# Optimization experiments

Hardware: AMD Instinct MI355X
Metric: run time of the kernel (lower is better)

## Reference

```python
import jax, jax.numpy as jnp
import numpy as np

EPS = 1e-07
B, C, K = 524288, 42, 8  # batch, n_channel, n_constituent
HID = [5, 4, 4]


def _make_net_params(key, n_in, lower=-1.0, upper=1.0):
    dims = [n_in] + HID + [3]
    params = []
    for i in range(4):
        key, kw, kb = jax.random.split(key, 3)
        W = jax.random.uniform(kw, (C, dims[i + 1], dims[i]), minval=lower, maxval=upper)
        if i < 3:  # hidden bias init 0.9..1.1
            b = jax.random.uniform(kb, (C, dims[i + 1]), minval=0.9, maxval=1.1)
        else:     # output bias init -0.1..0.1
            b = jax.random.uniform(kb, (C, dims[i + 1]), minval=-0.1, maxval=0.1)
        params.append(W)
        params.append(b)
    return params


def setup_inputs() -> dict:
    key = jax.random.key(0)
    k = jax.random.split(key, 6)
    inp = {
        'tau': jax.random.uniform(k[0], (B, C, K), dtype=jnp.float32),
        'mu_direct': jax.random.uniform(k[1], (B, 1), minval=0.01, maxval=1.0, dtype=jnp.float32),
        'mu_diffuse': jax.random.uniform(k[2], (B, 1), minval=0.01, maxval=1.0, dtype=jnp.float32),
        'constituents': jax.random.uniform(k[3], (B, K), dtype=jnp.float32),
    }
    dp = _make_net_params(k[4], K + 1)
    fp = _make_net_params(k[5], K)
    names = ['W1', 'b1', 'W2', 'b2', 'W3', 'b3', 'W4', 'b4']
    for n, p in zip(names, dp):
        inp['d' + n] = p
    for n, p in zip(names, fp):
        inp['f' + n] = p
    return inp


def _batched_mlp(x, W1, b1, W2, b2, W3, b3, W4, b4):
    # x: [B, n_in]; Wi: [C, out, in]; runs all C tiny MLPs at once (eval mode, dropout off)
    h = jax.nn.relu(jnp.einsum('bi,coi->bco', x, W1) + b1)        # [B,C,5]
    h = jax.nn.relu(jnp.einsum('bch,coh->bco', h, W2) + b2)       # [B,C,4]
    h = jax.nn.relu(jnp.einsum('bch,coh->bco', h, W3) + b3)       # [B,C,4]
    return jnp.einsum('bch,coh->bco', h, W4) + b4                 # [B,C,3]


def reference(tau, mu_direct, mu_diffuse, constituents,
              dW1, db1, dW2, db2, dW3, db3, dW4, db4,
              fW1, fb1, fW2, fb2, fW3, fb3, fW4, fb4):
    tau_total = jnp.sum(tau, axis=2)                              # [B,C]
    t_direct = jnp.exp(-tau_total / (mu_direct + EPS))
    t_diffuse = jnp.exp(-tau_total / (mu_diffuse + EPS))
    x_direct = jnp.concatenate([constituents / (mu_direct + EPS), mu_direct], axis=1)  # [B,K+1]
    e_split_direct = jax.nn.softmax(
        _batched_mlp(x_direct, dW1, db1, dW2, db2, dW3, db3, dW4, db4), axis=-1)       # [B,C,3]
    e_split_diffuse = jax.nn.softmax(
        _batched_mlp(constituents, fW1, fb1, fW2, fb2, fW3, fb3, fW4, fb4), axis=-1)   # [B,C,3]
    return (t_direct, t_diffuse, e_split_direct, e_split_diffuse)
```

## Files before the change

### kernel.cpp

```cpp
#include <hip/hip_runtime.h>

constexpr int Bn  = 524288;
constexpr int Cn  = 42;
constexpr int BC  = Bn * Cn;
constexpr int BC4 = BC / 4;
constexpr int QS  = 672;
constexpr int TS  = 4 * QS;
constexpr float EPSf = 1e-7f;

typedef float f4 __attribute__((ext_vector_type(4)));
struct F3 { float x, y, z; };

__device__ __forceinline__ float frcp(float x) { return __builtin_amdgcn_rcpf(x); }


__global__ __launch_bounds__(256) void scat_main(
    const float* __restrict__ tau,
    const float* __restrict__ mu_direct,
    const float* __restrict__ mu_diffuse,
    const float* __restrict__ cons,
    const float* __restrict__ dW1, const float* __restrict__ db1,
    const float* __restrict__ dW2, const float* __restrict__ db2,
    const float* __restrict__ dW3, const float* __restrict__ db3,
    const float* __restrict__ dW4, const float* __restrict__ db4,
    const float* __restrict__ fW1, const float* __restrict__ fb1,
    const float* __restrict__ fW2, const float* __restrict__ fb2,
    const float* __restrict__ fW3, const float* __restrict__ fb3,
    const float* __restrict__ fW4, const float* __restrict__ fb4,
    float* __restrict__ out)
{
    __shared__ float lds[213 * 42];

    auto stage = [&](const float* __restrict__ src, int n, int per_c, auto rowfn) {
        for (int i = threadIdx.x; i < n; i += 256) {
            int cc  = i / per_c;
            int rem = i - cc * per_c;
            lds[rowfn(rem) * 42 + cc] = src[i];
        }
    };
    stage(dW1, 1890, 45, [](int r) { return (r / 9) * 10 + (r % 9); });
    stage(db1,  210,  5, [](int r) { return r * 10 + 9; });
    stage(dW2,  840, 20, [](int r) { return 50 + (r / 5) * 6 + (r % 5); });
    stage(db2,  168,  4, [](int r) { return 50 + r * 6 + 5; });
    stage(dW3,  672, 16, [](int r) { return 74 + (r / 4) * 5 + (r % 4); });
    stage(db3,  168,  4, [](int r) { return 74 + r * 5 + 4; });
    stage(dW4,  504, 12, [](int r) { return 94 + (r / 4) * 5 + (r % 4); });
    stage(db4,  126,  3, [](int r) { return 94 + r * 5 + 4; });
    stage(fW1, 1680, 40, [](int r) { return 109 + (r / 8) * 9 + (r % 8); });
    stage(fb1,  210,  5, [](int r) { return 109 + r * 9 + 8; });
    stage(fW2,  840, 20, [](int r) { return 154 + (r / 5) * 6 + (r % 5); });
    stage(fb2,  168,  4, [](int r) { return 154 + r * 6 + 5; });
    stage(fW3,  672, 16, [](int r) { return 178 + (r / 4) * 5 + (r % 4); });
    stage(fb3,  168,  4, [](int r) { return 178 + r * 5 + 4; });
    stage(fW4,  504, 12, [](int r) { return 198 + (r / 4) * 5 + (r % 4); });
    stage(fb4,  126,  3, [](int r) { return 198 + r * 5 + 4; });
    __syncthreads();

    const int u    = blockIdx.x * 256 + threadIdx.x;
    const int tile = u / QS;
    const int lane = u - tile * QS;
    const int p0   = tile * TS + lane;
    const int c    = lane % Cn;
    const int b0   = p0 / Cn;
    const float* wc = lds + c;

    f4 ta[4], tb[4];
#pragma unroll
    for (int q = 0; q < 4; ++q) {
        const f4* t4 = reinterpret_cast<const f4*>(tau) + (p0 + q * QS) * 2;
        ta[q] = __builtin_nontemporal_load(t4);
        tb[q] = __builtin_nontemporal_load(t4 + 1);
    }

    float mud[4], muf[4], invd[4];
    float xc[4][8];
#pragma unroll
    for (int q = 0; q < 4; ++q) {
        const int bq = b0 + q * 16;
        float md = mu_direct[bq];
        muf[q] = mu_diffuse[bq];
        const f4* c4 = reinterpret_cast<const f4*>(cons) + bq * 2;
        f4 ca = c4[0], cb = c4[1];
        xc[q][0] = ca.x; xc[q][1] = ca.y; xc[q][2] = ca.z; xc[q][3] = ca.w;
        xc[q][4] = cb.x; xc[q][5] = cb.y; xc[q][6] = cb.z; xc[q][7] = cb.w;
        mud[q] = md; invd[q] = frcp(md + EPSf);
    }

    float h1[4][5], h2[4][4], h3[4][4], oo[4][3];

#pragma unroll
    for (int o = 0; o < 5; ++o) {
        float a0 = 0.f, a1 = 0.f, a2 = 0.f, a3 = 0.f;
#pragma unroll
        for (int i = 0; i < 8; ++i) {
            float w = wc[(109 + o * 9 + i) * 42];
            a0 = fmaf(w, xc[0][i], a0);
            a1 = fmaf(w, xc[1][i], a1);
            a2 = fmaf(w, xc[2][i], a2);
            a3 = fmaf(w, xc[3][i], a3);
        }
        float bs = wc[(109 + o * 9 + 8) * 42];
        h1[0][o] = fmaxf(a0 + bs, 0.f);
        h1[1][o] = fmaxf(a1 + bs, 0.f);
        h1[2][o] = fmaxf(a2 + bs, 0.f);
        h1[3][o] = fmaxf(a3 + bs, 0.f);
    }
#pragma unroll
    for (int o = 0; o < 4; ++o) {
        float a0 = 0.f, a1 = 0.f, a2 = 0.f, a3 = 0.f;
#pragma unroll
        for (int i = 0; i < 5; ++i) {
            float w = wc[(154 + o * 6 + i) * 42];
            a0 = fmaf(w, h1[0][i], a0);
            a1 = fmaf(w, h1[1][i], a1);
            a2 = fmaf(w, h1[2][i], a2);
            a3 = fmaf(w, h1[3][i], a3);
        }
        float bs = wc[(154 + o * 6 + 5) * 42];
        h2[0][o] = fmaxf(a0 + bs, 0.f);
        h2[1][o] = fmaxf(a1 + bs, 0.f);
        h2[2][o] = fmaxf(a2 + bs, 0.f);
        h2[3][o] = fmaxf(a3 + bs, 0.f);
    }
#pragma unroll
    for (int o = 0; o < 4; ++o) {
        float a0 = 0.f, a1 = 0.f, a2 = 0.f, a3 = 0.f;
#pragma unroll
        for (int i = 0; i < 4; ++i) {
            float w = wc[(178 + o * 5 + i) * 42];
            a0 = fmaf(w, h2[0][i], a0);
            a1 = fmaf(w, h2[1][i], a1);
            a2 = fmaf(w, h2[2][i], a2);
            a3 = fmaf(w, h2[3][i], a3);
        }
        float bs = wc[(178 + o * 5 + 4) * 42];
        h3[0][o] = fmaxf(a0 + bs, 0.f);
        h3[1][o] = fmaxf(a1 + bs, 0.f);
        h3[2][o] = fmaxf(a2 + bs, 0.f);
        h3[3][o] = fmaxf(a3 + bs, 0.f);
    }
#pragma unroll
    for (int o = 0; o < 3; ++o) {
        float a0 = 0.f, a1 = 0.f, a2 = 0.f, a3 = 0.f;
#pragma unroll
        for (int i = 0; i < 4; ++i) {
            float w = wc[(198 + o * 5 + i) * 42];
            a0 = fmaf(w, h3[0][i], a0);
            a1 = fmaf(w, h3[1][i], a1);
            a2 = fmaf(w, h3[2][i], a2);
            a3 = fmaf(w, h3[3][i], a3);
        }
        float bs = wc[(198 + o * 5 + 4) * 42];
        oo[0][o] = a0 + bs; oo[1][o] = a1 + bs; oo[2][o] = a2 + bs; oo[3][o] = a3 + bs;
    }
#pragma unroll
    for (int q = 0; q < 4; ++q) {
        float v0 = oo[q][0], v1 = oo[q][1], v2 = oo[q][2];
        float m = fmaxf(fmaxf(v0, v1), v2);
        float e0 = __expf(v0 - m), e1 = __expf(v1 - m), e2 = __expf(v2 - m);
        float rs = frcp(e0 + e1 + e2);
        F3 v; v.x = e0 * rs; v.y = e1 * rs; v.z = e2 * rs;
        *reinterpret_cast<F3*>(out + 5 * BC + (p0 + q * QS) * 3) = v;
    }

#pragma unroll
    for (int q = 0; q < 4; ++q)
#pragma unroll
        for (int i = 0; i < 8; ++i) xc[q][i] *= invd[q];

#pragma unroll
    for (int o = 0; o < 5; ++o) {
        float a0 = 0.f, a1 = 0.f, a2 = 0.f, a3 = 0.f;
#pragma unroll
        for (int i = 0; i < 9; ++i) {
            float w = wc[(o * 10 + i) * 42];
            float x0 = (i < 8) ? xc[0][i] : mud[0];
            float x1 = (i < 8) ? xc[1][i] : mud[1];
            float x2 = (i < 8) ? xc[2][i] : mud[2];
            float x3 = (i < 8) ? xc[3][i] : mud[3];
            a0 = fmaf(w, x0, a0);
            a1 = fmaf(w, x1, a1);
            a2 = fmaf(w, x2, a2);
            a3 = fmaf(w, x3, a3);
        }
        float bs = wc[(o * 10 + 9) * 42];
        h1[0][o] = fmaxf(a0 + bs, 0.f);
        h1[1][o] = fmaxf(a1 + bs, 0.f);
        h1[2][o] = fmaxf(a2 + bs, 0.f);
        h1[3][o] = fmaxf(a3 + bs, 0.f);
    }
#pragma unroll
    for (int o = 0; o < 4; ++o) {
        float a0 = 0.f, a1 = 0.f, a2 = 0.f, a3 = 0.f;
#pragma unroll
        for (int i = 0; i < 5; ++i) {
            float w = wc[(50 + o * 6 + i) * 42];
            a0 = fmaf(w, h1[0][i], a0);
            a1 = fmaf(w, h1[1][i], a1);
            a2 = fmaf(w, h1[2][i], a2);
            a3 = fmaf(w, h1[3][i], a3);
        }
        float bs = wc[(50 + o * 6 + 5) * 42];
        h2[0][o] = fmaxf(a0 + bs, 0.f);
        h2[1][o] = fmaxf(a1 + bs, 0.f);
        h2[2][o] = fmaxf(a2 + bs, 0.f);
        h2[3][o] = fmaxf(a3 + bs, 0.f);
    }
#pragma unroll
    for (int o = 0; o < 4; ++o) {
        float a0 = 0.f, a1 = 0.f, a2 = 0.f, a3 = 0.f;
#pragma unroll
        for (int i = 0; i < 4; ++i) {
            float w = wc[(74 + o * 5 + i) * 42];
            a0 = fmaf(w, h2[0][i], a0);
            a1 = fmaf(w, h2[1][i], a1);
            a2 = fmaf(w, h2[2][i], a2);
            a3 = fmaf(w, h2[3][i], a3);
        }
        float bs = wc[(74 + o * 5 + 4) * 42];
        h3[0][o] = fmaxf(a0 + bs, 0.f);
        h3[1][o] = fmaxf(a1 + bs, 0.f);
        h3[2][o] = fmaxf(a2 + bs, 0.f);
        h3[3][o] = fmaxf(a3 + bs, 0.f);
    }
#pragma unroll
    for (int o = 0; o < 3; ++o) {
        float a0 = 0.f, a1 = 0.f, a2 = 0.f, a3 = 0.f;
#pragma unroll
        for (int i = 0; i < 4; ++i) {
            float w = wc[(94 + o * 5 + i) * 42];
            a0 = fmaf(w, h3[0][i], a0);
            a1 = fmaf(w, h3[1][i], a1);
            a2 = fmaf(w, h3[2][i], a2);
            a3 = fmaf(w, h3[3][i], a3);
        }
        float bs = wc[(94 + o * 5 + 4) * 42];
        oo[0][o] = a0 + bs; oo[1][o] = a1 + bs; oo[2][o] = a2 + bs; oo[3][o] = a3 + bs;
    }
#pragma unroll
    for (int q = 0; q < 4; ++q) {
        float v0 = oo[q][0], v1 = oo[q][1], v2 = oo[q][2];
        float m = fmaxf(fmaxf(v0, v1), v2);
        float e0 = __expf(v0 - m), e1 = __expf(v1 - m), e2 = __expf(v2 - m);
        float rs = frcp(e0 + e1 + e2);
        F3 v; v.x = e0 * rs; v.y = e1 * rs; v.z = e2 * rs;
        *reinterpret_cast<F3*>(out + 2 * BC + (p0 + q * QS) * 3) = v;
    }

#pragma unroll
    for (int q = 0; q < 4; ++q) {
        const int pq = p0 + q * QS;
        f4 a = ta[q], b = tb[q];
        float tt = ((a.x + a.y) + (a.z + a.w)) + ((b.x + b.y) + (b.z + b.w));
        out[pq]      = __expf(-tt * invd[q]);
        out[BC + pq] = __expf(-tt * frcp(muf[q] + EPSf));
    }
}

extern "C" void kernel_launch(void* const* d_in, const int* in_sizes, int n_in,
                              void* d_out, int out_size, void* d_ws, size_t ws_size,
                              hipStream_t stream) {
    const float* tau  = (const float*)d_in[0];
    const float* mu_d = (const float*)d_in[1];
    const float* mu_f = (const float*)d_in[2];
    const float* cons = (const float*)d_in[3];

    dim3 grid(BC4 / 256);
    scat_main<<<grid, 256, 0, stream>>>(
        tau, mu_d, mu_f, cons,
        (const float*)d_in[4],  (const float*)d_in[5],
        (const float*)d_in[6],  (const float*)d_in[7],
        (const float*)d_in[8],  (const float*)d_in[9],
        (const float*)d_in[10], (const float*)d_in[11],
        (const float*)d_in[12], (const float*)d_in[13],
        (const float*)d_in[14], (const float*)d_in[15],
        (const float*)d_in[16], (const float*)d_in[17],
        (const float*)d_in[18], (const float*)d_in[19],
        (float*)d_out);
}
```

Measured before the change: 369.2 us.

## Split tau reduction into separate kernel and make MLP kernel persistent

Moves the tau row-sum into its own streaming kernel that writes the totals into the first output slot. A persistent MLP kernel then loops 16 tiles per block, so the weight staging into shared memory is paid once per block rather than once per 256 threads. The MLP kernel reads the staged tau totals back and overwrites them with the exp transmittances. The cost is an extra launch plus a write and re-read of a B*C float intermediate.

```diff
diff --git a/kernel.cpp b/kernel.cpp
--- a/kernel.cpp
+++ b/kernel.cpp
@@ -8,14 +8,30 @@
 constexpr int TS  = 4 * QS;
 constexpr float EPSf = 1e-7f;
 
+constexpr int MLP_BLOCKS = 1344;
+constexpr int MLP_ITERS  = 16;
+
 typedef float f4 __attribute__((ext_vector_type(4)));
 struct F3 { float x, y, z; };
 
 __device__ __forceinline__ float frcp(float x) { return __builtin_amdgcn_rcpf(x); }
 
-
-__global__ __launch_bounds__(256) void scat_main(
-    const float* __restrict__ tau,
+__global__ __launch_bounds__(256) void reduce_kernel(
+    const float* __restrict__ tau, float* __restrict__ out)
+{
+    const long t = blockIdx.x * 256 + threadIdx.x;
+    const f4* src = reinterpret_cast<const f4*>(tau) + t * 8;
+    f4 r;
+#pragma unroll
+    for (int q = 0; q < 4; ++q) {
+        f4 a = __builtin_nontemporal_load(src + 2 * q);
+        f4 b = __builtin_nontemporal_load(src + 2 * q + 1);
+        r[q] = ((a.x + a.y) + (a.z + a.w)) + ((b.x + b.y) + (b.z + b.w));
+    }
+    __builtin_nontemporal_store(r, reinterpret_cast<f4*>(out) + t);
+}
+
+__global__ __launch_bounds__(256) void mlp_kernel(
     const float* __restrict__ mu_direct,
     const float* __restrict__ mu_diffuse,
     const float* __restrict__ cons,
@@ -56,204 +72,201 @@
     stage(fb4,  126,  3, [](int r) { return 198 + r * 5 + 4; });
     __syncthreads();
 
-    const int u    = blockIdx.x * 256 + threadIdx.x;
-    const int tile = u / QS;
-    const int lane = u - tile * QS;
-    const int p0   = tile * TS + lane;
-    const int c    = lane % Cn;
-    const int b0   = p0 / Cn;
-    const float* wc = lds + c;
-
-    f4 ta[4], tb[4];
-#pragma unroll
-    for (int q = 0; q < 4; ++q) {
-        const f4* t4 = reinterpret_cast<const f4*>(tau) + (p0 + q * QS) * 2;
-        ta[q] = __builtin_nontemporal_load(t4);
-        tb[q] = __builtin_nontemporal_load(t4 + 1);
-    }
-
-    float mud[4], muf[4], invd[4];
-    float xc[4][8];
-#pragma unroll
-    for (int q = 0; q < 4; ++q) {
-        const int bq = b0 + q * 16;
-        float md = mu_direct[bq];
-        muf[q] = mu_diffuse[bq];
-        const f4* c4 = reinterpret_cast<const f4*>(cons) + bq * 2;
-        f4 ca = c4[0], cb = c4[1];
-        xc[q][0] = ca.x; xc[q][1] = ca.y; xc[q][2] = ca.z; xc[q][3] = ca.w;
-        xc[q][4] = cb.x; xc[q][5] = cb.y; xc[q][6] = cb.z; xc[q][7] = cb.w;
-        mud[q] = md; invd[q] = frcp(md + EPSf);
-    }
-
-    float h1[4][5], h2[4][4], h3[4][4], oo[4][3];
-
-#pragma unroll
-    for (int o = 0; o < 5; ++o) {
-        float a0 = 0.f, a1 = 0.f, a2 = 0.f, a3 = 0.f;
-#pragma unroll
-        for (int i = 0; i < 8; ++i) {
-            float w = wc[(109 + o * 9 + i) * 42];
-            a0 = fmaf(w, xc[0][i], a0);
-            a1 = fmaf(w, xc[1][i], a1);
-            a2 = fmaf(w, xc[2][i], a2);
-            a3 = fmaf(w, xc[3][i], a3);
-        }
-        float bs = wc[(109 + o * 9 + 8) * 42];
-        h1[0][o] = fmaxf(a0 + bs, 0.f);
-        h1[1][o] = fmaxf(a1 + bs, 0.f);
-        h1[2][o] = fmaxf(a2 + bs, 0.f);
-        h1[3][o] = fmaxf(a3 + bs, 0.f);
-    }
-#pragma unroll
-    for (int o = 0; o < 4; ++o) {
-        float a0 = 0.f, a1 = 0.f, a2 = 0.f, a3 = 0.f;
-#pragma unroll
-        for (int i = 0; i < 5; ++i) {
-            float w = wc[(154 + o * 6 + i) * 42];
-            a0 = fmaf(w, h1[0][i], a0);
-            a1 = fmaf(w, h1[1][i], a1);
-            a2 = fmaf(w, h1[2][i], a2);
-            a3 = fmaf(w, h1[3][i], a3);
-        }
-        float bs = wc[(154 + o * 6 + 5) * 42];
-        h2[0][o] = fmaxf(a0 + bs, 0.f);
-        h2[1][o] = fmaxf(a1 + bs, 0.f);
-        h2[2][o] = fmaxf(a2 + bs, 0.f);
-        h2[3][o] = fmaxf(a3 + bs, 0.f);
-    }
-#pragma unroll
-    for (int o = 0; o < 4; ++o) {
-        float a0 = 0.f, a1 = 0.f, a2 = 0.f, a3 = 0.f;
-#pragma unroll
-        for (int i = 0; i < 4; ++i) {
-            float w = wc[(178 + o * 5 + i) * 42];
-            a0 = fmaf(w, h2[0][i], a0);
-            a1 = fmaf(w, h2[1][i], a1);
-            a2 = fmaf(w, h2[2][i], a2);
-            a3 = fmaf(w, h2[3][i], a3);
-        }
-        float bs = wc[(178 + o * 5 + 4) * 42];
-        h3[0][o] = fmaxf(a0 + bs, 0.f);
-        h3[1][o] = fmaxf(a1 + bs, 0.f);
-        h3[2][o] = fmaxf(a2 + bs, 0.f);
-        h3[3][o] = fmaxf(a3 + bs, 0.f);
-    }
-#pragma unroll
-    for (int o = 0; o < 3; ++o) {
-        float a0 = 0.f, a1 = 0.f, a2 = 0.f, a3 = 0.f;
-#pragma unroll
-        for (int i = 0; i < 4; ++i) {
-            float w = wc[(198 + o * 5 + i) * 42];
-            a0 = fmaf(w, h3[0][i], a0);
-            a1 = fmaf(w, h3[1][i], a1);
-            a2 = fmaf(w, h3[2][i], a2);
-            a3 = fmaf(w, h3[3][i], a3);
-        }
-        float bs = wc[(198 + o * 5 + 4) * 42];
-        oo[0][o] = a0 + bs; oo[1][o] = a1 + bs; oo[2][o] = a2 + bs; oo[3][o] = a3 + bs;
-    }
-#pragma unroll
-    for (int q = 0; q < 4; ++q) {
-        float v0 = oo[q][0], v1 = oo[q][1], v2 = oo[q][2];
-        float m = fmaxf(fmaxf(v0, v1), v2);
-        float e0 = __expf(v0 - m), e1 = __expf(v1 - m), e2 = __expf(v2 - m);
-        float rs = frcp(e0 + e1 + e2);
-        F3 v; v.x = e0 * rs; v.y = e1 * rs; v.z = e2 * rs;
-        *reinterpret_cast<F3*>(out + 5 * BC + (p0 + q * QS) * 3) = v;
-    }
-
-#pragma unroll
-    for (int q = 0; q < 4; ++q)
-#pragma unroll
-        for (int i = 0; i < 8; ++i) xc[q][i] *= invd[q];
-
-#pragma unroll
-    for (int o = 0; o < 5; ++o) {
-        float a0 = 0.f, a1 = 0.f, a2 = 0.f, a3 = 0.f;
-#pragma unroll
-        for (int i = 0; i < 9; ++i) {
-            float w = wc[(o * 10 + i) * 42];
-            float x0 = (i < 8) ? xc[0][i] : mud[0];
-            float x1 = (i < 8) ? xc[1][i] : mud[1];
-            float x2 = (i < 8) ? xc[2][i] : mud[2];
-            float x3 = (i < 8) ? xc[3][i] : mud[3];
-            a0 = fmaf(w, x0, a0);
-            a1 = fmaf(w, x1, a1);
-            a2 = fmaf(w, x2, a2);
-            a3 = fmaf(w, x3, a3);
-        }
-        float bs = wc[(o * 10 + 9) * 42];
-        h1[0][o] = fmaxf(a0 + bs, 0.f);
-        h1[1][o] = fmaxf(a1 + bs, 0.f);
-        h1[2][o] = fmaxf(a2 + bs, 0.f);
-        h1[3][o] = fmaxf(a3 + bs, 0.f);
-    }
-#pragma unroll
-    for (int o = 0; o < 4; ++o) {
-        float a0 = 0.f, a1 = 0.f, a2 = 0.f, a3 = 0.f;
-#pragma unroll
-        for (int i = 0; i < 5; ++i) {
-            float w = wc[(50 + o * 6 + i) * 42];
-            a0 = fmaf(w, h1[0][i], a0);
-            a1 = fmaf(w, h1[1][i], a1);
-            a2 = fmaf(w, h1[2][i], a2);
-            a3 = fmaf(w, h1[3][i], a3);
-        }
-        float bs = wc[(50 + o * 6 + 5) * 42];
-        h2[0][o] = fmaxf(a0 + bs, 0.f);
-        h2[1][o] = fmaxf(a1 + bs, 0.f);
-        h2[2][o] = fmaxf(a2 + bs, 0.f);
-        h2[3][o] = fmaxf(a3 + bs, 0.f);
-    }
-#pragma unroll
-    for (int o = 0; o < 4; ++o) {
-        float a0 = 0.f, a1 = 0.f, a2 = 0.f, a3 = 0.f;
-#pragma unroll
-        for (int i = 0; i < 4; ++i) {
-            float w = wc[(74 + o * 5 + i) * 42];
-            a0 = fmaf(w, h2[0][i], a0);
-            a1 = fmaf(w, h2[1][i], a1);
-            a2 = fmaf(w, h2[2][i], a2);
-            a3 = fmaf(w, h2[3][i], a3);
-        }
-        float bs = wc[(74 + o * 5 + 4) * 42];
-        h3[0][o] = fmaxf(a0 + bs, 0.f);
-        h3[1][o] = fmaxf(a1 + bs, 0.f);
-        h3[2][o] = fmaxf(a2 + bs, 0.f);
-        h3[3][o] = fmaxf(a3 + bs, 0.f);
-    }
-#pragma unroll
-    for (int o = 0; o < 3; ++o) {
-        float a0 = 0.f, a1 = 0.f, a2 = 0.f, a3 = 0.f;
-#pragma unroll
-        for (int i = 0; i < 4; ++i) {
-            float w = wc[(94 + o * 5 + i) * 42];
-            a0 = fmaf(w, h3[0][i], a0);
-            a1 = fmaf(w, h3[1][i], a1);
-            a2 = fmaf(w, h3[2][i], a2);
-            a3 = fmaf(w, h3[3][i], a3);
-        }
-        float bs = wc[(94 + o * 5 + 4) * 42];
-        oo[0][o] = a0 + bs; oo[1][o] = a1 + bs; oo[2][o] = a2 + bs; oo[3][o] = a3 + bs;
-    }
-#pragma unroll
-    for (int q = 0; q < 4; ++q) {
-        float v0 = oo[q][0], v1 = oo[q][1], v2 = oo[q][2];
-        float m = fmaxf(fmaxf(v0, v1), v2);
-        float e0 = __expf(v0 - m), e1 = __expf(v1 - m), e2 = __expf(v2 - m);
-        float rs = frcp(e0 + e1 + e2);
-        F3 v; v.x = e0 * rs; v.y = e1 * rs; v.z = e2 * rs;
-        *reinterpret_cast<F3*>(out + 2 * BC + (p0 + q * QS) * 3) = v;
-    }
-
-#pragma unroll
-    for (int q = 0; q < 4; ++q) {
-        const int pq = p0 + q * QS;
-        f4 a = ta[q], b = tb[q];
-        float tt = ((a.x + a.y) + (a.z + a.w)) + ((b.x + b.y) + (b.z + b.w));
-        out[pq]      = __expf(-tt * invd[q]);
-        out[BC + pq] = __expf(-tt * frcp(muf[q] + EPSf));
+#pragma unroll 1
+    for (int it = 0; it < MLP_ITERS; ++it) {
+        const int u    = (blockIdx.x * MLP_ITERS + it) * 256 + threadIdx.x;
+        const int tile = u / QS;
+        const int lane = u - tile * QS;
+        const int p0   = tile * TS + lane;
+        const int c    = lane % Cn;
+        const int b0   = p0 / Cn;
+        const float* wc = lds + c;
+
+        float tt[4];
+#pragma unroll
+        for (int q = 0; q < 4; ++q) tt[q] = out[p0 + q * QS];
+
+        float mud[4], muf[4], invd[4];
+        float xc[4][8];
+#pragma unroll
+        for (int q = 0; q < 4; ++q) {
+            const int bq = b0 + q * 16;
+            float md = mu_direct[bq];
+            muf[q] = mu_diffuse[bq];
+            const f4* c4 = reinterpret_cast<const f4*>(cons) + bq * 2;
+            f4 ca = c4[0], cb = c4[1];
+            xc[q][0] = ca.x; xc[q][1] = ca.y; xc[q][2] = ca.z; xc[q][3] = ca.w;
+            xc[q][4] = cb.x; xc[q][5] = cb.y; xc[q][6] = cb.z; xc[q][7] = cb.w;
+            mud[q] = md; invd[q] = frcp(md + EPSf);
+        }
+
+        float h1[4][5], h2[4][4], h3[4][4], oo[4][3];
+
+#pragma unroll
+        for (int o = 0; o < 5; ++o) {
+            float a0 = 0.f, a1 = 0.f, a2 = 0.f, a3 = 0.f;
+#pragma unroll
+            for (int i = 0; i < 8; ++i) {
+                float w = wc[(109 + o * 9 + i) * 42];
+                a0 = fmaf(w, xc[0][i], a0);
+                a1 = fmaf(w, xc[1][i], a1);
+                a2 = fmaf(w, xc[2][i], a2);
+                a3 = fmaf(w, xc[3][i], a3);
+            }
+            float bs = wc[(109 + o * 9 + 8) * 42];
+            h1[0][o] = fmaxf(a0 + bs, 0.f);
+            h1[1][o] = fmaxf(a1 + bs, 0.f);
+            h1[2][o] = fmaxf(a2 + bs, 0.f);
+            h1[3][o] = fmaxf(a3 + bs, 0.f);
+        }
+#pragma unroll
+        for (int o = 0; o < 4; ++o) {
+            float a0 = 0.f, a1 = 0.f, a2 = 0.f, a3 = 0.f;
+#pragma unroll
+            for (int i = 0; i < 5; ++i) {
+                float w = wc[(154 + o * 6 + i) * 42];
+                a0 = fmaf(w, h1[0][i], a0);
+                a1 = fmaf(w, h1[1][i], a1);
+                a2 = fmaf(w, h1[2][i], a2);
+                a3 = fmaf(w, h1[3][i], a3);
+            }
+            float bs = wc[(154 + o * 6 + 5) * 42];
+            h2[0][o] = fmaxf(a0 + bs, 0.f);
+            h2[1][o] = fmaxf(a1 + bs, 0.f);
+            h2[2][o] = fmaxf(a2 + bs, 0.f);
+            h2[3][o] = fmaxf(a3 + bs, 0.f);
+        }
+#pragma unroll
+        for (int o = 0; o < 4; ++o) {
+            float a0 = 0.f, a1 = 0.f, a2 = 0.f, a3 = 0.f;
+#pragma unroll
+            for (int i = 0; i < 4; ++i) {
+                float w = wc[(178 + o * 5 + i) * 42];
+                a0 = fmaf(w, h2[0][i], a0);
+                a1 = fmaf(w, h2[1][i], a1);
+                a2 = fmaf(w, h2[2][i], a2);
+                a3 = fmaf(w, h2[3][i], a3);
+            }
+            float bs = wc[(178 + o * 5 + 4) * 42];
+            h3[0][o] = fmaxf(a0 + bs, 0.f);
+            h3[1][o] = fmaxf(a1 + bs, 0.f);
+            h3[2][o] = fmaxf(a2 + bs, 0.f);
+            h3[3][o] = fmaxf(a3 + bs, 0.f);
+        }
+#pragma unroll
+        for (int o = 0; o < 3; ++o) {
+            float a0 = 0.f, a1 = 0.f, a2 = 0.f, a3 = 0.f;
+#pragma unroll
+            for (int i = 0; i < 4; ++i) {
+                float w = wc[(198 + o * 5 + i) * 42];
+                a0 = fmaf(w, h3[0][i], a0);
+                a1 = fmaf(w, h3[1][i], a1);
+                a2 = fmaf(w, h3[2][i], a2);
+                a3 = fmaf(w, h3[3][i], a3);
+            }
+            float bs = wc[(198 + o * 5 + 4) * 42];
+            oo[0][o] = a0 + bs; oo[1][o] = a1 + bs; oo[2][o] = a2 + bs; oo[3][o] = a3 + bs;
+        }
+#pragma unroll
+        for (int q = 0; q < 4; ++q) {
+            float v0 = oo[q][0], v1 = oo[q][1], v2 = oo[q][2];
+            float m = fmaxf(fmaxf(v0, v1), v2);
+            float e0 = __expf(v0 - m), e1 = __expf(v1 - m), e2 = __expf(v2 - m);
+            float rs = frcp(e0 + e1 + e2);
+            F3 v; v.x = e0 * rs; v.y = e1 * rs; v.z = e2 * rs;
+            *reinterpret_cast<F3*>(out + 5 * BC + (p0 + q * QS) * 3) = v;
+        }
+
+#pragma unroll
+        for (int q = 0; q < 4; ++q)
+#pragma unroll
+            for (int i = 0; i < 8; ++i) xc[q][i] *= invd[q];
+
+#pragma unroll
+        for (int o = 0; o < 5; ++o) {
+            float a0 = 0.f, a1 = 0.f, a2 = 0.f, a3 = 0.f;
+#pragma unroll
+            for (int i = 0; i < 9; ++i) {
+                float w = wc[(o * 10 + i) * 42];
+                float x0 = (i < 8) ? xc[0][i] : mud[0];
+                float x1 = (i < 8) ? xc[1][i] : mud[1];
+                float x2 = (i < 8) ? xc[2][i] : mud[2];
+                float x3 = (i < 8) ? xc[3][i] : mud[3];
+                a0 = fmaf(w, x0, a0);
+                a1 = fmaf(w, x1, a1);
+                a2 = fmaf(w, x2, a2);
+                a3 = fmaf(w, x3, a3);
+            }
+            float bs = wc[(o * 10 + 9) * 42];
+            h1[0][o] = fmaxf(a0 + bs, 0.f);
+            h1[1][o] = fmaxf(a1 + bs, 0.f);
+            h1[2][o] = fmaxf(a2 + bs, 0.f);
+            h1[3][o] = fmaxf(a3 + bs, 0.f);
+        }
+#pragma unroll
+        for (int o = 0; o < 4; ++o) {
+            float a0 = 0.f, a1 = 0.f, a2 = 0.f, a3 = 0.f;
+#pragma unroll
+            for (int i = 0; i < 5; ++i) {
+                float w = wc[(50 + o * 6 + i) * 42];
+                a0 = fmaf(w, h1[0][i], a0);
+                a1 = fmaf(w, h1[1][i], a1);
+                a2 = fmaf(w, h1[2][i], a2);
+                a3 = fmaf(w, h1[3][i], a3);
+            }
+            float bs = wc[(50 + o * 6 + 5) * 42];
+            h2[0][o] = fmaxf(a0 + bs, 0.f);
+            h2[1][o] = fmaxf(a1 + bs, 0.f);
+            h2[2][o] = fmaxf(a2 + bs, 0.f);
+            h2[3][o] = fmaxf(a3 + bs, 0.f);
+        }
+#pragma unroll
+        for (int o = 0; o < 4; ++o) {
+            float a0 = 0.f, a1 = 0.f, a2 = 0.f, a3 = 0.f;
+#pragma unroll
+            for (int i = 0; i < 4; ++i) {
+                float w = wc[(74 + o * 5 + i) * 42];
+                a0 = fmaf(w, h2[0][i], a0);
+                a1 = fmaf(w, h2[1][i], a1);
+                a2 = fmaf(w, h2[2][i], a2);
+                a3 = fmaf(w, h2[3][i], a3);
+            }
+            float bs = wc[(74 + o * 5 + 4) * 42];
+            h3[0][o] = fmaxf(a0 + bs, 0.f);
+            h3[1][o] = fmaxf(a1 + bs, 0.f);
+            h3[2][o] = fmaxf(a2 + bs, 0.f);
+            h3[3][o] = fmaxf(a3 + bs, 0.f);
+        }
+#pragma unroll
+        for (int o = 0; o < 3; ++o) {
+            float a0 = 0.f, a1 = 0.f, a2 = 0.f, a3 = 0.f;
+#pragma unroll
+            for (int i = 0; i < 4; ++i) {
+                float w = wc[(94 + o * 5 + i) * 42];
+                a0 = fmaf(w, h3[0][i], a0);
+                a1 = fmaf(w, h3[1][i], a1);
+                a2 = fmaf(w, h3[2][i], a2);
+                a3 = fmaf(w, h3[3][i], a3);
+            }
+            float bs = wc[(94 + o * 5 + 4) * 42];
+            oo[0][o] = a0 + bs; oo[1][o] = a1 + bs; oo[2][o] = a2 + bs; oo[3][o] = a3 + bs;
+        }
+#pragma unroll
+        for (int q = 0; q < 4; ++q) {
+            float v0 = oo[q][0], v1 = oo[q][1], v2 = oo[q][2];
+            float m = fmaxf(fmaxf(v0, v1), v2);
+            float e0 = __expf(v0 - m), e1 = __expf(v1 - m), e2 = __expf(v2 - m);
+            float rs = frcp(e0 + e1 + e2);
+            F3 v; v.x = e0 * rs; v.y = e1 * rs; v.z = e2 * rs;
+            *reinterpret_cast<F3*>(out + 2 * BC + (p0 + q * QS) * 3) = v;
+        }
+
+#pragma unroll
+        for (int q = 0; q < 4; ++q) {
+            const int pq = p0 + q * QS;
+            out[pq]      = __expf(-tt[q] * invd[q]);
+            out[BC + pq] = __expf(-tt[q] * frcp(muf[q] + EPSf));
+        }
     }
 }
 
@@ -265,9 +278,10 @@
     const float* mu_f = (const float*)d_in[2];
     const float* cons = (const float*)d_in[3];
 
-    dim3 grid(BC4 / 256);
-    scat_main<<<grid, 256, 0, stream>>>(
-        tau, mu_d, mu_f, cons,
+    reduce_kernel<<<dim3(BC4 / 256), 256, 0, stream>>>(tau, (float*)d_out);
+
+    mlp_kernel<<<dim3(MLP_BLOCKS), 256, 0, stream>>>(
+        mu_d, mu_f, cons,
         (const float*)d_in[4],  (const float*)d_in[5],
         (const float*)d_in[6],  (const float*)d_in[7],
         (const float*)d_in[8],  (const float*)d_in[9],
```

After: 573.2 us. 55.3% more time.
